# Performance work log

Measured on AMD Instinct MI355X. Metric: run time of the kernel, lower is better.

The kernel has to match this reference:

```python
import jax, jax.numpy as jnp
import numpy as np

VOCAB = 5000
HID = 256
BATCH = 64
STEPS = 256


def setup_inputs() -> dict:
    key = jax.random.key(0)
    ks = jax.random.split(key, 7)
    scale_k = 1.0 / np.sqrt(VOCAB)
    scale_r = 1.0 / np.sqrt(HID)
    return {
        "tokens": jax.random.randint(ks[0], (BATCH, STEPS), 0, VOCAB, dtype=jnp.int32),
        "h0": jnp.zeros((BATCH, HID), dtype=jnp.float32),
        # GRUCell params (Keras reset_after=True layout): kernel [V,3H], recurrent [H,3H], bias [2,3H]
        "kernel": jax.random.normal(ks[1], (VOCAB, 3 * HID), dtype=jnp.float32) * scale_k,
        "rkernel": jax.random.normal(ks[2], (HID, 3 * HID), dtype=jnp.float32) * scale_r,
        "bias": jnp.zeros((2, 3 * HID), dtype=jnp.float32),
        # final Dense(vocab_size)
        "Wd": jax.random.normal(ks[3], (HID, VOCAB), dtype=jnp.float32) * scale_r,
        "bd": jnp.zeros((VOCAB,), dtype=jnp.float32),
    }


def reference(tokens, h0, kernel, rkernel, bias, Wd, bd):
    # X = one_hot(transpose(inputs), vocab)  -> time-major [T, B, V]
    X = jax.nn.one_hot(tokens.T, VOCAB, dtype=kernel.dtype)

    b_in, b_rec = bias[0], bias[1]

    def step(h, x):  # x: [B, V], h: [B, H]
        mx = x @ kernel + b_in            # [B, 3H]
        mh = h @ rkernel + b_rec          # [B, 3H]
        xz, xr, xh = jnp.split(mx, 3, axis=-1)
        hz, hr, hh = jnp.split(mh, 3, axis=-1)
        z = jax.nn.sigmoid(xz + hz)
        r = jax.nn.sigmoid(xr + hr)
        cand = jnp.tanh(xh + r * hh)      # reset_after=True candidate
        h_new = z * h + (1.0 - z) * cand
        return h_new, h_new

    h_last, Y = jax.lax.scan(step, h0, X)  # Y: [T, B, H]
    out = Y.reshape(-1, Y.shape[-1]) @ Wd + bd  # [T*B, V]
    return out, h_last
```

## Files before the change

### kernel.cpp

```cpp
#include <hip/hip_runtime.h>
#include <cstdint>

typedef __attribute__((ext_vector_type(8))) short bf16x8;
typedef __attribute__((ext_vector_type(4))) float f32x4;
typedef unsigned short u16;
typedef unsigned int u32;

#define T_STEPS 256
#define BATCH 64
#define HID 256
#define VOCAB 5000
#define KC 768
#define NWG 16
#define HB 16
#define NPAD 5120

__device__ __forceinline__ u16 f2bf(float x) {
  union { float f; u32 u; } v; v.f = x;
  u32 r = v.u + 0x7fffu + ((v.u >> 16) & 1u);
  return (u16)(r >> 16);
}
__device__ __forceinline__ float bf2f(u16 b) {
  union { float f; u32 u; } v; v.u = ((u32)b) << 16;
  return v.f;
}
__device__ __forceinline__ void load_lds16(const void* g, void* l) {
  __builtin_amdgcn_global_load_lds(
      (const __attribute__((address_space(1))) void*)g,
      (__attribute__((address_space(3))) void*)l, 16, 0, 0);
}

__global__ __launch_bounds__(256) void prep_b(const float* __restrict__ Wd,
                                              u16* __restrict__ BT) {
  int gid = blockIdx.x * 256 + threadIdx.x;
  int n = gid / 96;
  int k0 = (gid % 96) * 8;
  union { uint4 q; u16 s[8]; } o;
#pragma unroll
  for (int i = 0; i < 8; ++i) {
    int k = k0 + i;
    float x = 0.f;
    if (n < VOCAB) {
      int kk = (k < 512) ? (k & 255) : (k - 512);
      x = Wd[kk * VOCAB + n];
    }
    u16 hi = f2bf(x);
    o.s[i] = (k < 512) ? hi : f2bf(x - bf2f(hi));
  }
  *(uint4*)(BT + (size_t)n * KC + k0) = o.q;
}

__global__ __launch_bounds__(256) void prep_h0(const float* __restrict__ h0,
                                               u16* __restrict__ H0S) {
  int i = blockIdx.x * 256 + threadIdx.x;
  int b = i >> 8, j = i & 255;
  float x = h0[i];
  u16 hi = f2bf(x);
  u16 lo = f2bf(x - bf2f(hi));
  H0S[b * KC + j] = hi;
  H0S[b * KC + 256 + j] = lo;
}

__global__ __launch_bounds__(256, 1) void gru_rec(
    const int* __restrict__ tokens, const float* __restrict__ h0,
    const float* __restrict__ ker, const float* __restrict__ rker,
    const float* __restrict__ bias,
    u16* __restrict__ Abuf, const u16* __restrict__ H0S,
    float* __restrict__ hlast, u32* __restrict__ flags) {
  const int g = blockIdx.x;
  const int tid = threadIdx.x;
  const int w = tid >> 6;
  const int l = tid & 63;
  const int lm = l & 15;
  const int lq = l >> 4;

  int cmap[3]; float brec[3], bin[3];
#pragma unroll
  for (int nt = 0; nt < 3; ++nt) {
    cmap[nt] = nt * 256 + g * HB + lm;
    bin[nt]  = bias[cmap[nt]];
    brec[nt] = bias[KC + cmap[nt]];
  }

  bf16x8 Bhi[3][8], Blo[3][8];
#pragma unroll
  for (int nt = 0; nt < 3; ++nt)
#pragma unroll
    for (int kb = 0; kb < 8; ++kb) {
      union { bf16x8 v; u16 s[8]; } uh, ul;
#pragma unroll
      for (int jj = 0; jj < 8; ++jj) {
        int k = kb * 32 + lq * 8 + jj;
        float x = rker[k * KC + cmap[nt]];
        u16 hi = f2bf(x);
        uh.s[jj] = hi;
        ul.s[jj] = f2bf(x - bf2f(hi));
      }
      Bhi[nt][kb] = uh.v; Blo[nt][kb] = ul.v;
    }

  float hown[4];
#pragma unroll
  for (int r = 0; r < 4; ++r)
    hown[r] = h0[(16 * w + lq * 4 + r) * HID + g * HB + lm];

  const int rowloc = 16 * w + lm;

  for (int t = 0; t < T_STEPS; ++t) {
    float mx[3][4];
#pragma unroll
    for (int r = 0; r < 4; ++r) {
      int b = 16 * w + lq * 4 + r;
      int tok = tokens[b * T_STEPS + t];
#pragma unroll
      for (int nt = 0; nt < 3; ++nt)
        mx[nt][r] = ker[(size_t)tok * KC + cmap[nt]] + bin[nt];
    }

    if (t > 0) {
      const u32 tt = (u32)t;
      int guard = 0;
      for (;;) {
        u32 v = __hip_atomic_load(&flags[(l & 15) * 32], __ATOMIC_RELAXED,
                                  __HIP_MEMORY_SCOPE_AGENT);
        if (__all((int)(v >= tt))) break;
        if (++guard > (1 << 24)) break;
        __builtin_amdgcn_s_sleep(1);
      }
      __threadfence();
    }

    const u16* hsrc = (t == 0) ? H0S : (Abuf + (size_t)(t - 1) * BATCH * KC);
    const u16* hrow = hsrc + (size_t)rowloc * KC;
    bf16x8 Ahi[8], Alo[8];
#pragma unroll
    for (int kb = 0; kb < 8; ++kb) {
      union { uint4 q; bf16x8 v; } a0, a1;
      a0.q = *(const uint4*)(hrow + kb * 32 + lq * 8);
      a1.q = *(const uint4*)(hrow + 256 + kb * 32 + lq * 8);
      Ahi[kb] = a0.v; Alo[kb] = a1.v;
    }

    f32x4 acc[3];
#pragma unroll
    for (int nt = 0; nt < 3; ++nt)
      acc[nt] = (f32x4){brec[nt], brec[nt], brec[nt], brec[nt]};

#pragma unroll
    for (int kb = 0; kb < 8; ++kb) {
#pragma unroll
      for (int nt = 0; nt < 3; ++nt) {
        acc[nt] = __builtin_amdgcn_mfma_f32_16x16x32_bf16(Ahi[kb], Bhi[nt][kb], acc[nt], 0, 0, 0);
        acc[nt] = __builtin_amdgcn_mfma_f32_16x16x32_bf16(Alo[kb], Bhi[nt][kb], acc[nt], 0, 0, 0);
        acc[nt] = __builtin_amdgcn_mfma_f32_16x16x32_bf16(Ahi[kb], Blo[nt][kb], acc[nt], 0, 0, 0);
      }
    }

#pragma unroll
    for (int r = 0; r < 4; ++r) {
      float z  = 1.f / (1.f + expf(-(acc[0][r] + mx[0][r])));
      float rr = 1.f / (1.f + expf(-(acc[1][r] + mx[1][r])));
      float cd = tanhf(mx[2][r] + rr * acc[2][r]);
      float hn = z * hown[r] + (1.f - z) * cd;
      hown[r] = hn;
      u16 hi = f2bf(hn);
      u16 lo = f2bf(hn - bf2f(hi));
      int b = 16 * w + lq * 4 + r;
      u16* orow = Abuf + (size_t)(t * BATCH + b) * KC;
      orow[g * HB + lm]       = hi;
      orow[256 + g * HB + lm] = lo;
      orow[512 + g * HB + lm] = hi;
    }

    __threadfence();
    __syncthreads();
    if (tid == 0)
      __hip_atomic_store(&flags[g * 32], (u32)(t + 1), __ATOMIC_RELEASE,
                         __HIP_MEMORY_SCOPE_AGENT);
  }

#pragma unroll
  for (int r = 0; r < 4; ++r) {
    int b = 16 * w + lq * 4 + r;
    hlast[b * HID + g * HB + lm] = hown[r];
  }
}

__global__ __launch_bounds__(256, 2) void gemm_out(
    const u16* __restrict__ A, const u16* __restrict__ BT,
    const float* __restrict__ bd, float* __restrict__ out) {
  __shared__ u16 As[128 * 32];
  __shared__ u16 Bs[128 * 32];
  const int tid = threadIdx.x;
  const int w = tid >> 6, l = tid & 63;
  const int lm = l & 15, lq = l >> 4;
  const int wm = w & 1, wn = w >> 1;
  const int m0 = blockIdx.y * 128;
  const int n0 = blockIdx.x * 128;
  const int tr = tid >> 2;
  const int tc = (tid & 3) * 8;

  f32x4 acc[4][4] = {};

  for (int kb = 0; kb < 24; ++kb) {
    if (kb) __syncthreads();
#pragma unroll
    for (int j = 0; j < 2; ++j) {
      load_lds16(A  + (size_t)(m0 + j * 64 + tr) * KC + kb * 32 + tc,
                 As + j * 2048 + (tid >> 6) * 512);
      load_lds16(BT + (size_t)(n0 + j * 64 + tr) * KC + kb * 32 + tc,
                 Bs + j * 2048 + (tid >> 6) * 512);
    }
    __syncthreads();

    bf16x8 af[4], bfr[4];
#pragma unroll
    for (int mi = 0; mi < 4; ++mi)
      af[mi] = *(const bf16x8*)(As + (wm * 64 + mi * 16 + lm) * 32 + lq * 8);
#pragma unroll
    for (int ni = 0; ni < 4; ++ni)
      bfr[ni] = *(const bf16x8*)(Bs + (wn * 64 + ni * 16 + lm) * 32 + lq * 8);
#pragma unroll
    for (int mi = 0; mi < 4; ++mi)
#pragma unroll
      for (int ni = 0; ni < 4; ++ni)
        acc[mi][ni] = __builtin_amdgcn_mfma_f32_16x16x32_bf16(af[mi], bfr[ni], acc[mi][ni], 0, 0, 0);
  }

#pragma unroll
  for (int ni = 0; ni < 4; ++ni) {
    int n = n0 + wn * 64 + ni * 16 + lm;
    float bdv = (n < VOCAB) ? bd[n] : 0.f;
#pragma unroll
    for (int mi = 0; mi < 4; ++mi) {
#pragma unroll
      for (int r = 0; r < 4; ++r) {
        int m = m0 + wm * 64 + mi * 16 + lq * 4 + r;
        if (n < VOCAB) out[(size_t)m * VOCAB + n] = acc[mi][ni][r] + bdv;
      }
    }
  }
}

extern "C" void kernel_launch(void* const* d_in, const int* in_sizes, int n_in,
                              void* d_out, int out_size, void* d_ws, size_t ws_size,
                              hipStream_t stream) {
  const int*   tokens = (const int*)d_in[0];
  const float* h0     = (const float*)d_in[1];
  const float* ker    = (const float*)d_in[2];
  const float* rker   = (const float*)d_in[3];
  const float* bias   = (const float*)d_in[4];
  const float* Wd     = (const float*)d_in[5];
  const float* bd     = (const float*)d_in[6];
  float* out = (float*)d_out;
  char* ws = (char*)d_ws;

  u16* Abuf  = (u16*)(ws);
  u16* BT    = (u16*)(ws + 25165824);
  u16* H0S   = (u16*)(ws + 33030144);
  u32* flags = (u32*)(ws + 33128448);

  hipMemsetAsync(flags, 0, 2048, stream);
  prep_b<<<1920, 256, 0, stream>>>(Wd, BT);
  prep_h0<<<64, 256, 0, stream>>>(h0, H0S);
  gru_rec<<<NWG, 256, 0, stream>>>(tokens, h0, ker, rker, bias, Abuf, H0S,
                                   out + (size_t)16384 * VOCAB, flags);
  gemm_out<<<dim3(40, 128), 256, 0, stream>>>(Abuf, BT, bd, out);
}
```

Measured before the change: 2.301 ms.

## Pack hi/lo bf16 hidden state, swizzle layouts, prefetch embeddings, cheaper activations

The hidden-state buffer now packs hi/lo bf16 pairs into one u32 per element, stored with an XOR swizzle. This drops the duplicated third copy and shrinks the recurrent read and write traffic. The recurrent loop replaces the heavy threadfences with atomic relaxed stores and loads, prefetches the next step's embedding rows after signalling the flag, and uses fast __expf-based sigmoid and tanh. The output GEMM runs 8 k-blocks with three MFMAs each, unpacking hi/lo from LDS and reading swizzled B tiles. The relaxed memory ordering and the approximate transcendentals risk subtle correctness or precision issues.

Result: slower. 2.426 ms (+5.4%).

```diff
diff --git a/kernel.cpp b/kernel.cpp
--- a/kernel.cpp
+++ b/kernel.cpp
@@ -5,6 +5,7 @@
 typedef __attribute__((ext_vector_type(4))) float f32x4;
 typedef unsigned short u16;
 typedef unsigned int u32;
+typedef unsigned long long u64;
 
 #define T_STEPS 256
 #define BATCH 64
@@ -12,8 +13,6 @@
 #define VOCAB 5000
 #define KC 768
 #define NWG 16
-#define HB 16
-#define NPAD 5120
 
 __device__ __forceinline__ u16 f2bf(float x) {
   union { float f; u32 u; } v; v.f = x;
@@ -24,48 +23,59 @@
   union { float f; u32 u; } v; v.u = ((u32)b) << 16;
   return v.f;
 }
+__device__ __forceinline__ u32 packhl(float x) {
+  u16 hi = f2bf(x);
+  u16 lo = f2bf(x - bf2f(hi));
+  return (u32)hi | ((u32)lo << 16);
+}
 __device__ __forceinline__ void load_lds16(const void* g, void* l) {
   __builtin_amdgcn_global_load_lds(
       (const __attribute__((address_space(1))) void*)g,
       (__attribute__((address_space(3))) void*)l, 16, 0, 0);
 }
+__device__ __forceinline__ u64 ald64(const u32* p) {
+  return __hip_atomic_load((const u64*)p, __ATOMIC_RELAXED, __HIP_MEMORY_SCOPE_AGENT);
+}
+__device__ __forceinline__ float sigm(float x) { return 1.f / (1.f + __expf(-x)); }
+__device__ __forceinline__ float tanh_f(float x) {
+  return 2.f / (1.f + __expf(-2.f * x)) - 1.f;
+}
 
 __global__ __launch_bounds__(256) void prep_b(const float* __restrict__ Wd,
                                               u16* __restrict__ BT) {
   int gid = blockIdx.x * 256 + threadIdx.x;
-  int n = gid / 96;
-  int k0 = (gid % 96) * 8;
+  int segp = gid / 5120;
+  int n = gid % 5120;
+  int blk = segp >> 2, sp = segp & 3;
+  int sl = sp ^ ((n >> 1) & 3);
+  int cl = (blk * 4 + sl) * 8;
   union { uint4 q; u16 s[8]; } o;
 #pragma unroll
   for (int i = 0; i < 8; ++i) {
-    int k = k0 + i;
-    float x = 0.f;
-    if (n < VOCAB) {
-      int kk = (k < 512) ? (k & 255) : (k - 512);
-      x = Wd[kk * VOCAB + n];
-    }
+    int c = cl + i;
+    int k = c & 255;
+    float x = (n < VOCAB) ? Wd[k * VOCAB + n] : 0.f;
     u16 hi = f2bf(x);
-    o.s[i] = (k < 512) ? hi : f2bf(x - bf2f(hi));
-  }
-  *(uint4*)(BT + (size_t)n * KC + k0) = o.q;
+    o.s[i] = (c < 256) ? hi : f2bf(x - bf2f(hi));
+  }
+  *(uint4*)(BT + (size_t)n * 512 + segp * 8) = o.q;
 }
 
 __global__ __launch_bounds__(256) void prep_h0(const float* __restrict__ h0,
-                                               u16* __restrict__ H0S) {
+                                               u32* __restrict__ H0S) {
   int i = blockIdx.x * 256 + threadIdx.x;
   int b = i >> 8, j = i & 255;
-  float x = h0[i];
-  u16 hi = f2bf(x);
-  u16 lo = f2bf(x - bf2f(hi));
-  H0S[b * KC + j] = hi;
-  H0S[b * KC + 256 + j] = lo;
+  u32 val = packhl(h0[i]);
+  int segG = j >> 2;
+  int segS = (segG & ~7) | ((segG & 7) ^ (b & 7));
+  H0S[(size_t)b * 256 + segS * 4 + (j & 3)] = val;
 }
 
 __global__ __launch_bounds__(256, 1) void gru_rec(
     const int* __restrict__ tokens, const float* __restrict__ h0,
     const float* __restrict__ ker, const float* __restrict__ rker,
     const float* __restrict__ bias,
-    u16* __restrict__ Abuf, const u16* __restrict__ H0S,
+    u32* __restrict__ AbufP, const u32* __restrict__ H0S,
     float* __restrict__ hlast, u32* __restrict__ flags) {
   const int g = blockIdx.x;
   const int tid = threadIdx.x;
@@ -73,11 +83,12 @@
   const int l = tid & 63;
   const int lm = l & 15;
   const int lq = l >> 4;
+  const int r7 = lm & 7;
 
   int cmap[3]; float brec[3], bin[3];
 #pragma unroll
   for (int nt = 0; nt < 3; ++nt) {
-    cmap[nt] = nt * 256 + g * HB + lm;
+    cmap[nt] = nt * 256 + g * 16 + lm;
     bin[nt]  = bias[cmap[nt]];
     brec[nt] = bias[KC + cmap[nt]];
   }
@@ -102,43 +113,44 @@
   float hown[4];
 #pragma unroll
   for (int r = 0; r < 4; ++r)
-    hown[r] = h0[(16 * w + lq * 4 + r) * HID + g * HB + lm];
-
-  const int rowloc = 16 * w + lm;
+    hown[r] = h0[(16 * w + lq * 4 + r) * HID + g * 16 + lm];
+
+  float mx[3][4];
+#pragma unroll
+  for (int r = 0; r < 4; ++r) {
+    int b = 16 * w + lq * 4 + r;
+    int tok = tokens[b * T_STEPS + 0];
+#pragma unroll
+    for (int nt = 0; nt < 3; ++nt)
+      mx[nt][r] = ker[(size_t)tok * KC + cmap[nt]] + bin[nt];
+  }
 
   for (int t = 0; t < T_STEPS; ++t) {
-    float mx[3][4];
-#pragma unroll
-    for (int r = 0; r < 4; ++r) {
-      int b = 16 * w + lq * 4 + r;
-      int tok = tokens[b * T_STEPS + t];
-#pragma unroll
-      for (int nt = 0; nt < 3; ++nt)
-        mx[nt][r] = ker[(size_t)tok * KC + cmap[nt]] + bin[nt];
-    }
-
     if (t > 0) {
       const u32 tt = (u32)t;
       int guard = 0;
       for (;;) {
-        u32 v = __hip_atomic_load(&flags[(l & 15) * 32], __ATOMIC_RELAXED,
-                                  __HIP_MEMORY_SCOPE_AGENT);
+        u32 v = tt;
+        if (l < 16)
+          v = __hip_atomic_load(&flags[l * 32], __ATOMIC_RELAXED,
+                                __HIP_MEMORY_SCOPE_AGENT);
         if (__all((int)(v >= tt))) break;
         if (++guard > (1 << 24)) break;
         __builtin_amdgcn_s_sleep(1);
       }
-      __threadfence();
-    }
-
-    const u16* hsrc = (t == 0) ? H0S : (Abuf + (size_t)(t - 1) * BATCH * KC);
-    const u16* hrow = hsrc + (size_t)rowloc * KC;
-    bf16x8 Ahi[8], Alo[8];
+    }
+
+    const u32* src = ((t == 0) ? H0S : (AbufP + (size_t)(t - 1) * BATCH * 256))
+                     + (size_t)(16 * w + lm) * 256;
+    u64 raw[32];
 #pragma unroll
     for (int kb = 0; kb < 8; ++kb) {
-      union { uint4 q; bf16x8 v; } a0, a1;
-      a0.q = *(const uint4*)(hrow + kb * 32 + lq * 8);
-      a1.q = *(const uint4*)(hrow + 256 + kb * 32 + lq * 8);
-      Ahi[kb] = a0.v; Alo[kb] = a1.v;
+      int s0 = kb * 8 + ((lq * 2) ^ r7);
+      int s1 = kb * 8 + (((lq * 2) | 1) ^ r7);
+      raw[kb * 4 + 0] = ald64(src + s0 * 4);
+      raw[kb * 4 + 1] = ald64(src + s0 * 4 + 2);
+      raw[kb * 4 + 2] = ald64(src + s1 * 4);
+      raw[kb * 4 + 3] = ald64(src + s1 * 4 + 2);
     }
 
     f32x4 acc[3];
@@ -148,83 +160,130 @@
 
 #pragma unroll
     for (int kb = 0; kb < 8; ++kb) {
+      u32 p[8];
+      p[0] = (u32)raw[kb * 4 + 0]; p[1] = (u32)(raw[kb * 4 + 0] >> 32);
+      p[2] = (u32)raw[kb * 4 + 1]; p[3] = (u32)(raw[kb * 4 + 1] >> 32);
+      p[4] = (u32)raw[kb * 4 + 2]; p[5] = (u32)(raw[kb * 4 + 2] >> 32);
+      p[6] = (u32)raw[kb * 4 + 3]; p[7] = (u32)(raw[kb * 4 + 3] >> 32);
+      union { u32 u[4]; bf16x8 v; } hi, lo;
+#pragma unroll
+      for (int i = 0; i < 4; ++i) {
+        hi.u[i] = (p[2 * i] & 0xffffu) | (p[2 * i + 1] << 16);
+        lo.u[i] = (p[2 * i] >> 16) | (p[2 * i + 1] & 0xffff0000u);
+      }
 #pragma unroll
       for (int nt = 0; nt < 3; ++nt) {
-        acc[nt] = __builtin_amdgcn_mfma_f32_16x16x32_bf16(Ahi[kb], Bhi[nt][kb], acc[nt], 0, 0, 0);
-        acc[nt] = __builtin_amdgcn_mfma_f32_16x16x32_bf16(Alo[kb], Bhi[nt][kb], acc[nt], 0, 0, 0);
-        acc[nt] = __builtin_amdgcn_mfma_f32_16x16x32_bf16(Ahi[kb], Blo[nt][kb], acc[nt], 0, 0, 0);
+        acc[nt] = __builtin_amdgcn_mfma_f32_16x16x32_bf16(hi.v, Bhi[nt][kb], acc[nt], 0, 0, 0);
+        acc[nt] = __builtin_amdgcn_mfma_f32_16x16x32_bf16(lo.v, Bhi[nt][kb], acc[nt], 0, 0, 0);
+        acc[nt] = __builtin_amdgcn_mfma_f32_16x16x32_bf16(hi.v, Blo[nt][kb], acc[nt], 0, 0, 0);
       }
     }
 
 #pragma unroll
     for (int r = 0; r < 4; ++r) {
-      float z  = 1.f / (1.f + expf(-(acc[0][r] + mx[0][r])));
-      float rr = 1.f / (1.f + expf(-(acc[1][r] + mx[1][r])));
-      float cd = tanhf(mx[2][r] + rr * acc[2][r]);
+      float z  = sigm(acc[0][r] + mx[0][r]);
+      float rg = sigm(acc[1][r] + mx[1][r]);
+      float cd = tanh_f(mx[2][r] + rg * acc[2][r]);
       float hn = z * hown[r] + (1.f - z) * cd;
       hown[r] = hn;
-      u16 hi = f2bf(hn);
-      u16 lo = f2bf(hn - bf2f(hi));
       int b = 16 * w + lq * 4 + r;
-      u16* orow = Abuf + (size_t)(t * BATCH + b) * KC;
-      orow[g * HB + lm]       = hi;
-      orow[256 + g * HB + lm] = lo;
-      orow[512 + g * HB + lm] = hi;
-    }
-
-    __threadfence();
+      int segG = g * 4 + (lm >> 2);
+      int segS = (segG & ~7) | ((segG & 7) ^ (b & 7));
+      __hip_atomic_store(AbufP + (size_t)(t * BATCH + b) * 256 + segS * 4 + (lm & 3),
+                         packhl(hn), __ATOMIC_RELAXED, __HIP_MEMORY_SCOPE_AGENT);
+    }
+
     __syncthreads();
     if (tid == 0)
       __hip_atomic_store(&flags[g * 32], (u32)(t + 1), __ATOMIC_RELEASE,
                          __HIP_MEMORY_SCOPE_AGENT);
+
+    if (t + 1 < T_STEPS) {
+#pragma unroll
+      for (int r = 0; r < 4; ++r) {
+        int b = 16 * w + lq * 4 + r;
+        int tok = tokens[b * T_STEPS + t + 1];
+#pragma unroll
+        for (int nt = 0; nt < 3; ++nt)
+          mx[nt][r] = ker[(size_t)tok * KC + cmap[nt]] + bin[nt];
+      }
+    }
   }
 
 #pragma unroll
   for (int r = 0; r < 4; ++r) {
     int b = 16 * w + lq * 4 + r;
-    hlast[b * HID + g * HB + lm] = hown[r];
+    hlast[b * HID + g * 16 + lm] = hown[r];
   }
 }
 
 __global__ __launch_bounds__(256, 2) void gemm_out(
-    const u16* __restrict__ A, const u16* __restrict__ BT,
+    const u32* __restrict__ A, const u16* __restrict__ BT,
     const float* __restrict__ bd, float* __restrict__ out) {
-  __shared__ u16 As[128 * 32];
-  __shared__ u16 Bs[128 * 32];
+  __shared__ u32 Ap[128 * 32];
+  __shared__ u16 Bh[128 * 32];
+  __shared__ u16 Bl[128 * 32];
   const int tid = threadIdx.x;
   const int w = tid >> 6, l = tid & 63;
   const int lm = l & 15, lq = l >> 4;
   const int wm = w & 1, wn = w >> 1;
   const int m0 = blockIdx.y * 128;
   const int n0 = blockIdx.x * 128;
-  const int tr = tid >> 2;
-  const int tc = (tid & 3) * 8;
+  const int r7 = lm & 7;
+  const int b3 = (lm >> 1) & 3;
 
   f32x4 acc[4][4] = {};
 
-  for (int kb = 0; kb < 24; ++kb) {
+  for (int kb = 0; kb < 8; ++kb) {
     if (kb) __syncthreads();
 #pragma unroll
-    for (int j = 0; j < 2; ++j) {
-      load_lds16(A  + (size_t)(m0 + j * 64 + tr) * KC + kb * 32 + tc,
-                 As + j * 2048 + (tid >> 6) * 512);
-      load_lds16(BT + (size_t)(n0 + j * 64 + tr) * KC + kb * 32 + tc,
-                 Bs + j * 2048 + (tid >> 6) * 512);
+    for (int p = 0; p < 4; ++p) {
+      int c = p * 256 + tid;
+      int row = c >> 3, seg = c & 7;
+      load_lds16(A + (size_t)(m0 + row) * 256 + kb * 32 + seg * 4, Ap + c * 4);
+    }
+#pragma unroll
+    for (int p = 0; p < 2; ++p) {
+      int c = p * 256 + tid;
+      int row = c >> 2, sg = c & 3;
+      const u16* bsrc = BT + (size_t)(n0 + row) * 512 + kb * 32 + sg * 8;
+      load_lds16(bsrc, Bh + c * 8);
+      load_lds16(bsrc + 256, Bl + c * 8);
     }
     __syncthreads();
 
-    bf16x8 af[4], bfr[4];
+    bf16x8 ah[4], al[4], bh[4], bl[4];
+#pragma unroll
+    for (int mi = 0; mi < 4; ++mi) {
+      int row = wm * 64 + mi * 16 + lm;
+      int ls0 = (lq * 2) ^ r7;
+      int ls1 = ls0 ^ 1;
+      uint4 q0 = *(const uint4*)(Ap + row * 32 + ls0 * 4);
+      uint4 q1 = *(const uint4*)(Ap + row * 32 + ls1 * 4);
+      u32 p[8] = {q0.x, q0.y, q0.z, q0.w, q1.x, q1.y, q1.z, q1.w};
+      union { u32 u[4]; bf16x8 v; } hi, lo;
+#pragma unroll
+      for (int i = 0; i < 4; ++i) {
+        hi.u[i] = (p[2 * i] & 0xffffu) | (p[2 * i + 1] << 16);
+        lo.u[i] = (p[2 * i] >> 16) | (p[2 * i + 1] & 0xffff0000u);
+      }
+      ah[mi] = hi.v; al[mi] = lo.v;
+    }
+#pragma unroll
+    for (int ni = 0; ni < 4; ++ni) {
+      int row = wn * 64 + ni * 16 + lm;
+      int ls = lq ^ b3;
+      bh[ni] = *(const bf16x8*)(Bh + row * 32 + ls * 8);
+      bl[ni] = *(const bf16x8*)(Bl + row * 32 + ls * 8);
+    }
 #pragma unroll
     for (int mi = 0; mi < 4; ++mi)
-      af[mi] = *(const bf16x8*)(As + (wm * 64 + mi * 16 + lm) * 32 + lq * 8);
-#pragma unroll
-    for (int ni = 0; ni < 4; ++ni)
-      bfr[ni] = *(const bf16x8*)(Bs + (wn * 64 + ni * 16 + lm) * 32 + lq * 8);
-#pragma unroll
-    for (int mi = 0; mi < 4; ++mi)
-#pragma unroll
-      for (int ni = 0; ni < 4; ++ni)
-        acc[mi][ni] = __builtin_amdgcn_mfma_f32_16x16x32_bf16(af[mi], bfr[ni], acc[mi][ni], 0, 0, 0);
+#pragma unroll
+      for (int ni = 0; ni < 4; ++ni) {
+        acc[mi][ni] = __builtin_amdgcn_mfma_f32_16x16x32_bf16(ah[mi], bh[ni], acc[mi][ni], 0, 0, 0);
+        acc[mi][ni] = __builtin_amdgcn_mfma_f32_16x16x32_bf16(al[mi], bh[ni], acc[mi][ni], 0, 0, 0);
+        acc[mi][ni] = __builtin_amdgcn_mfma_f32_16x16x32_bf16(ah[mi], bl[ni], acc[mi][ni], 0, 0, 0);
+      }
   }
 
 #pragma unroll
@@ -255,15 +314,15 @@
   float* out = (float*)d_out;
   char* ws = (char*)d_ws;
 
-  u16* Abuf  = (u16*)(ws);
-  u16* BT    = (u16*)(ws + 25165824);
-  u16* H0S   = (u16*)(ws + 33030144);
-  u32* flags = (u32*)(ws + 33128448);
+  u32* AbufP = (u32*)(ws);
+  u16* BT    = (u16*)(ws + 16777216);
+  u32* H0S   = (u32*)(ws + 22020096);
+  u32* flags = (u32*)(ws + 22085632);
 
   hipMemsetAsync(flags, 0, 2048, stream);
-  prep_b<<<1920, 256, 0, stream>>>(Wd, BT);
+  prep_b<<<1280, 256, 0, stream>>>(Wd, BT);
   prep_h0<<<64, 256, 0, stream>>>(h0, H0S);
-  gru_rec<<<NWG, 256, 0, stream>>>(tokens, h0, ker, rker, bias, Abuf, H0S,
+  gru_rec<<<NWG, 256, 0, stream>>>(tokens, h0, ker, rker, bias, AbufP, H0S,
                                    out + (size_t)16384 * VOCAB, flags);
-  gemm_out<<<dim3(40, 128), 256, 0, stream>>>(Abuf, BT, bd, out);
-}
+  gemm_out<<<dim3(40, 128), 256, 0, stream>>>(AbufP, BT, bd, out);
+}
```
